# Performance work log

Measured on AMD Instinct MI355X. Metric: run time of the kernel, lower is better.

## Reference

```python
import jax, jax.numpy as jnp
import numpy as np

N = 50000
E = 640000
H = 128

def setup_inputs() -> dict:
    key = jax.random.key(0)
    ks = jax.random.split(key, 12)
    def lin(kw, fan_in, fan_out):
        # torch nn.Linear default init: U(-1/sqrt(fan_in), 1/sqrt(fan_in))
        lim = 1.0 / np.sqrt(fan_in)
        return jax.random.uniform(kw, (fan_in, fan_out), jnp.float32, -lim, lim)
    def bias(kb, fan_in, fan_out):
        lim = 1.0 / np.sqrt(fan_in)
        return jax.random.uniform(kb, (fan_out,), jnp.float32, -lim, lim)
    return {
        "x": jax.random.normal(ks[0], (N, H), jnp.float32),
        "pos": jax.random.normal(ks[1], (N, 3), jnp.float32),
        "edge_index": jax.random.randint(ks[2], (2, E), 0, N, jnp.int64),
        "msg_w1": lin(ks[3], 2 * H + 1, H), "msg_b1": bias(ks[4], 2 * H + 1, H),
        "msg_w2": lin(ks[5], H, H),         "msg_b2": bias(ks[6], H, H),
        "upd_w1": lin(ks[7], 2 * H, H),     "upd_b1": bias(ks[8], 2 * H, H),
        "upd_w2": lin(ks[9], H, H),         "upd_b2": bias(ks[10], H, H),
    }

def reference(x, pos, edge_index, msg_w1, msg_b1, msg_w2, msg_b2,
              upd_w1, upd_b1, upd_w2, upd_b2):
    send, rec = edge_index[0], edge_index[1]
    # pairwise distance per edge: [E]
    dist = jnp.linalg.norm(pos[send] - pos[rec], axis=1)
    # per-edge state: [E, 2H+1]
    state = jnp.concatenate([x[send], x[rec], dist[:, None]], axis=1)
    # message MLP: Linear -> SiLU -> Linear -> SiLU
    h = jax.nn.silu(state @ msg_w1 + msg_b1)
    message = jax.nn.silu(h @ msg_w2 + msg_b2)  # [E, H]
    # scatter-add into receiving nodes: [N, H]
    aggr = jax.ops.segment_sum(message, rec, num_segments=x.shape[0])
    # update MLP: Linear -> SiLU -> Linear
    u = jax.nn.silu(jnp.concatenate([x, aggr], axis=1) @ upd_w1 + upd_b1)
    update = u @ upd_w2 + upd_b2
    return update
```

## Files before the change

### kernel.cpp

```cpp
#include <hip/hip_runtime.h>
#include <math.h>

#define H 128

typedef unsigned short u16;
typedef unsigned int u32;
typedef __attribute__((ext_vector_type(4))) u32 u32x4;
typedef __attribute__((ext_vector_type(8))) __bf16 bf16x8;
typedef __attribute__((ext_vector_type(4))) float f32x4;
typedef __attribute__((ext_vector_type(16))) float f32x16;

union Frag { u32x4 u; bf16x8 b; };

__device__ __forceinline__ u32 pack2(float lo, float hi) {
    union { __bf16 b[2]; u32 u; } v;
    v.b[0] = (__bf16)lo; v.b[1] = (__bf16)hi;
    return v.u;
}
__device__ __forceinline__ float bflo(u32 w) {
    union { u32 i; float f; } v; v.i = w << 16; return v.f;
}
__device__ __forceinline__ float bfhi(u32 w) {
    union { u32 i; float f; } v; v.i = w & 0xffff0000u; return v.f;
}
__device__ __forceinline__ float silu(float v) {
    float e = __expf(-v);
    return v * __builtin_amdgcn_rcpf(1.0f + e);
}
__device__ __forceinline__ bf16x8 f8frag(float4 lo, float4 hi) {
    Frag f;
    f.u = (u32x4){pack2(lo.x, lo.y), pack2(lo.z, lo.w),
                  pack2(hi.x, hi.y), pack2(hi.z, hi.w)};
    return f.b;
}
__device__ __forceinline__ f32x16 mfma(bf16x8 a, bf16x8 b, f32x16 c) {
    return __builtin_amdgcn_mfma_f32_32x32x16_bf16(a, b, c, 0, 0, 0);
}
__device__ __forceinline__ f32x4 mfma16(bf16x8 a, bf16x8 b, f32x4 c) {
    return __builtin_amdgcn_mfma_f32_16x16x32_bf16(a, b, c, 0, 0, 0);
}
#define DPP_RADD(v, ctrl) \
    (v) += __int_as_float(__builtin_amdgcn_update_dpp(0, __float_as_int(v), (ctrl), 0xf, 0xf, 1))

__global__ void prep_kernel(const float* __restrict__ mw1, const float* __restrict__ mb1,
                            const float* __restrict__ mw2, const float* __restrict__ mb2,
                            const float* __restrict__ uw1, const float* __restrict__ ub1,
                            const float* __restrict__ uw2, const float* __restrict__ ub2,
                            u32* __restrict__ ws) {
    int t = blockIdx.x * blockDim.x + threadIdx.x;
    if (t >= 15936) return;
    if (t >= 15872) {
        int i = t - 15872;
        ws[63488 + i] = pack2(mw1[256 * H + 2 * i], mw1[256 * H + 2 * i + 1]);
        return;
    }
    if (t >= 13312) {
        int slot = t - 13312;
        int lane = slot & 63, fb = slot >> 6;
        int kb = fb >> 3, mt = fb & 7;
        int m = mt * 16 + (lane & 15);
        int quad = lane >> 4;
        u32 out[4];
        #pragma unroll
        for (int p = 0; p < 4; ++p) {
            float v[2];
            #pragma unroll
            for (int h = 0; h < 2; ++h) {
                int k = kb * 32 + quad * 8 + p * 2 + h;
                float val = 0.0f;
                if (k < 128)       val = mw2[(size_t)k * H + m];
                else if (k == 128) val = mb2[m];
                v[h] = val;
            }
            out[p] = pack2(v[0], v[1]);
        }
        u32* dst = ws + 53248 + (size_t)slot * 4;
        dst[0] = out[0]; dst[1] = out[1]; dst[2] = out[2]; dst[3] = out[3];
        return;
    }
    const float *W, *s0, *s1;
    int nK, slot, base;
    if (t < 4352)       { W = mw1; s0 = mw1 + 256 * H; s1 = mb1; nK = 256; slot = t;         base = 0;     }
    else if (t < 6656)  { W = mw2; s0 = mb2; s1 = nullptr;       nK = 128; slot = t - 4352;  base = 17408; }
    else if (t < 11008) { W = uw1; s0 = ub1; s1 = nullptr;       nK = 256; slot = t - 6656;  base = 26624; }
    else                { W = uw2; s0 = ub2; s1 = nullptr;       nK = 128; slot = t - 11008; base = 44032; }
    int lane = slot & 63, fb = slot >> 6;
    int ct, kb;
    if (nK == 256) { ct = fb / 17; kb = fb % 17; }
    else           { ct = fb / 9;  kb = fb % 9;  }
    int m = ct * 32 + (lane & 31);
    int q = lane >> 5;
    u32 out[4];
    #pragma unroll
    for (int p = 0; p < 4; ++p) {
        float v[2];
        #pragma unroll
        for (int h = 0; h < 2; ++h) {
            int k = kb * 16 + q * 8 + p * 2 + h;
            float val = 0.0f;
            if (k < nK)            val = W[(size_t)k * H + m];
            else if (k == nK)      val = s0 ? s0[m] : 0.0f;
            else if (k == nK + 1)  val = s1 ? s1[m] : 0.0f;
            v[h] = val;
        }
        out[p] = pack2(v[0], v[1]);
    }
    u32* dst = ws + base + (size_t)slot * 4;
    dst[0] = out[0]; dst[1] = out[1]; dst[2] = out[2]; dst[3] = out[3];
}

__global__ __launch_bounds__(256, 2) void front_kernel(
    const float* __restrict__ x, const u32* __restrict__ mw1s,
    u32* __restrict__ Pb, u32* __restrict__ Qb,
    const float* __restrict__ pos, const int* __restrict__ ei,
    int* __restrict__ deg, int2* __restrict__ bucket,
    int N, int E, int nIter, int PQB, int BKB)
{
    const int b = blockIdx.x;
    if (b < 2 * PQB) {
        const int isQ = (b >= PQB);
        const int bb = isQ ? (b - PQB) : b;
        const int kbBase = isQ ? 8 : 0;
        u32* outb = isQ ? Qb : Pb;

        const int lane = threadIdx.x & 63;
        const int q = lane >> 5, el = lane & 31;
        const int gw  = bb * 4 + (threadIdx.x >> 6);
        const int gws = PQB * 4;

        for (int it = gw; it < nIter; it += gws) {
            const int nA = it * 32 + el;
            const int ncA = (nA < N) ? nA : (N - 1);
            const float* xA = x + (size_t)ncA * H;

            f32x16 acc[4];
            #pragma unroll
            for (int ct = 0; ct < 4; ++ct) acc[ct] = (f32x16)0.0f;

            #pragma unroll
            for (int kb = 0; kb < 8; ++kb) {
                const int f = kb * 16 + q * 8;
                bf16x8 bA = f8frag(*(const float4*)(xA + f), *(const float4*)(xA + f + 4));
                #pragma unroll
                for (int ct = 0; ct < 4; ++ct) {
                    Frag a; a.u = *(const u32x4*)&mw1s[((size_t)(ct * 17 + kbBase + kb) * 64 + lane) * 4];
                    acc[ct] = mfma(a.b, bA, acc[ct]);
                }
            }
            if (isQ) {
                Frag bp; bp.u = (u32x4){0, 0, 0, 0};
                if (q == 0) bp.u.x = pack2(0.0f, 1.0f);
                #pragma unroll
                for (int ct = 0; ct < 4; ++ct) {
                    Frag a; a.u = *(const u32x4*)&mw1s[((size_t)(ct * 17 + 16) * 64 + lane) * 4];
                    acc[ct] = mfma(a.b, bp.b, acc[ct]);
                }
            }
            if (nA < N) {
                u32* prow = outb + (size_t)nA * 64;
                #pragma unroll
                for (int ct = 0; ct < 4; ++ct)
                    #pragma unroll
                    for (int g = 0; g < 4; ++g) {
                        u32 a = pack2(acc[ct][4*g + 0], acc[ct][4*g + 1]);
                        u32 bb2 = pack2(acc[ct][4*g + 2], acc[ct][4*g + 3]);
                        *(uint2*)(prow + ct * 16 + 4 * g + 2 * q) = make_uint2(a, bb2);
                    }
            }
        }
    } else {
        const int bb = b - 2 * PQB;
        for (int e = bb * 256 + (int)threadIdx.x; e < E; e += BKB * 256) {
            const int s = ei[e];
            const int r = ei[E + e];
            const float dx = pos[s*3]   - pos[r*3];
            const float dy = pos[s*3+1] - pos[r*3+1];
            const float dz = pos[s*3+2] - pos[r*3+2];
            const float dist = sqrtf(dx*dx + dy*dy + dz*dz);
            int slot = atomicAdd(&deg[r], 1);
            if (slot < 64) bucket[(size_t)r * 64 + slot] = make_int2(s, __float_as_int(dist));
        }
    }
}

__global__ __launch_bounds__(256, 3) void aggregate_kernel(
    const u32* __restrict__ Pbf, const u32* __restrict__ Qbf,
    const u32* __restrict__ wdp, const u32* __restrict__ ws16,
    const float* __restrict__ mb2,
    const int* __restrict__ deg, const int2* __restrict__ bucket,
    float* __restrict__ out, int N)
{
    __shared__ u32x4 af[2048];
    __shared__ float b2s[128];
    __shared__ u32x4 wds[16];
    for (int i = threadIdx.x; i < 2048; i += 256) af[i] = ((const u32x4*)ws16)[i];
    for (int i = threadIdx.x; i < 128; i += 256) b2s[i] = mb2[i];
    if (threadIdx.x < 16) wds[threadIdx.x] = ((const u32x4*)wdp)[threadIdx.x];
    __syncthreads();

    const int lane = threadIdx.x & 63;
    const int quad = lane >> 4, col = lane & 15;

    const int gw  = blockIdx.x * 4 + (threadIdx.x >> 6);
    const int gws = gridDim.x * 4;

    for (int n = gw; n < N; n += gws) {
        int dn = deg[n]; dn = (dn > 64) ? 64 : dn;
        const int nt = (dn + 15) >> 4;
        const u32x4* Qrow = (const u32x4*)(Qbf + (size_t)n * 64);

        f32x4 sum[8];
        #pragma unroll
        for (int mt = 0; mt < 8; ++mt) sum[mt] = (f32x4){0.f, 0.f, 0.f, 0.f};

        for (int t = 0; t < nt; ++t) {
            const int eIdx = t * 16 + col;
            const bool valid = eIdx < dn;
            const int eC = valid ? eIdx : (dn - 1);
            const int2 rec = bucket[(size_t)n * 64 + eC];
            const u32x4* Prow = (const u32x4*)(Pbf + (size_t)rec.x * 64);
            const float dist = __int_as_float(rec.y);

            f32x4 acc[8];
            #pragma unroll
            for (int mt = 0; mt < 8; ++mt)
                acc[mt] = *(const f32x4*)&b2s[mt * 16 + quad * 4];

            #pragma unroll 2
            for (int kb = 0; kb < 4; ++kb) {
                const u32x4 pc = Prow[kb * 4 + quad];
                const u32x4 qc = Qrow[kb * 4 + quad];
                const u32x4 wc = wds[kb * 4 + quad];
                const float v0 = silu(bflo(pc.x) + bflo(qc.x) + dist * bflo(wc.x));
                const float v1 = silu(bfhi(pc.x) + bfhi(qc.x) + dist * bfhi(wc.x));
                const float v2 = silu(bflo(pc.y) + bflo(qc.y) + dist * bflo(wc.y));
                const float v3 = silu(bfhi(pc.y) + bfhi(qc.y) + dist * bfhi(wc.y));
                const float v4 = silu(bflo(pc.z) + bflo(qc.z) + dist * bflo(wc.z));
                const float v5 = silu(bfhi(pc.z) + bfhi(qc.z) + dist * bfhi(wc.z));
                const float v6 = silu(bflo(pc.w) + bflo(qc.w) + dist * bflo(wc.w));
                const float v7 = silu(bfhi(pc.w) + bfhi(qc.w) + dist * bfhi(wc.w));
                Frag bf;
                bf.u = (u32x4){pack2(v0, v1), pack2(v2, v3), pack2(v4, v5), pack2(v6, v7)};
                if (!valid) bf.u = (u32x4){0, 0, 0, 0};
                #pragma unroll
                for (int mt = 0; mt < 8; ++mt) {
                    Frag a; a.u = af[(kb * 8 + mt) * 64 + lane];
                    acc[mt] = mfma16(a.b, bf.b, acc[mt]);
                }
            }
            #pragma unroll
            for (int mt = 0; mt < 8; ++mt) {
                sum[mt][0] += valid ? silu(acc[mt][0]) : 0.0f;
                sum[mt][1] += valid ? silu(acc[mt][1]) : 0.0f;
                sum[mt][2] += valid ? silu(acc[mt][2]) : 0.0f;
                sum[mt][3] += valid ? silu(acc[mt][3]) : 0.0f;
            }
        }

        #pragma unroll
        for (int mt = 0; mt < 8; ++mt)
            #pragma unroll
            for (int r = 0; r < 4; ++r) {
                float v = sum[mt][r];
                DPP_RADD(v, 0x128);
                DPP_RADD(v, 0x124);
                DPP_RADD(v, 0x122);
                DPP_RADD(v, 0x121);
                sum[mt][r] = v;
            }
        if (col == 0) {
            float* orow = out + (size_t)n * H;
            #pragma unroll
            for (int mt = 0; mt < 8; ++mt) {
                float4 v = { sum[mt][0], sum[mt][1], sum[mt][2], sum[mt][3] };
                *(float4*)(orow + mt * 16 + quad * 4) = v;
            }
        }
    }
}

__global__ __launch_bounds__(256, 2) void node1_kernel(
    const float* __restrict__ x, const float* __restrict__ aggr,
    const u32* __restrict__ ws, u32* __restrict__ Hb, int N, int nIter)
{
    __shared__ u32 lds[16384];
    const u32* wsl1 = ws + 26624;
    {
        const u32x4* src = (const u32x4*)wsl1;
        u32x4* dst = (u32x4*)lds;
        for (int i = threadIdx.x; i < 4096; i += 256) {
            int ln = i & 63, fb = i >> 6, ct = fb >> 4, kb = fb & 15;
            dst[i] = src[(ct * 17 + kb) * 64 + ln];
        }
    }
    __syncthreads();

    const int lane = threadIdx.x & 63;
    const int q = lane >> 5, el = lane & 31;
    const int gw  = blockIdx.x * 4 + (threadIdx.x >> 6);
    const int gws = gridDim.x * 4;

    for (int it = gw; it < nIter; it += gws) {
        const int nA = it * 32 + el;
        const int ncA = (nA < N) ? nA : (N - 1);
        const float* xA = x + (size_t)ncA * H;
        const float* gA = aggr + (size_t)ncA * H;

        f32x16 acc[4];
        #pragma unroll
        for (int ct = 0; ct < 4; ++ct) acc[ct] = (f32x16)0.0f;

        #pragma unroll
        for (int kb = 0; kb < 16; ++kb) {
            const int f = kb * 16 + q * 8;
            const float* pA = (f < H) ? (xA + f) : (gA + f - H);
            bf16x8 bA = f8frag(*(const float4*)pA, *(const float4*)(pA + 4));
            #pragma unroll
            for (int ct = 0; ct < 4; ++ct) {
                Frag a; a.u = *(const u32x4*)&lds[((ct * 16 + kb) * 64 + lane) * 4];
                acc[ct] = mfma(a.b, bA, acc[ct]);
            }
        }
        {
            Frag bp; bp.u = (u32x4){0,0,0,0};
            if (q == 0) bp.u.x = 0x00003F80u;
            #pragma unroll
            for (int ct = 0; ct < 4; ++ct) {
                Frag a; a.u = *(const u32x4*)&wsl1[((size_t)(ct * 17 + 16) * 64 + lane) * 4];
                acc[ct] = mfma(a.b, bp.b, acc[ct]);
            }
        }
        if (nA < N) {
            u32* hrow = Hb + (size_t)nA * 64;
            #pragma unroll
            for (int ct = 0; ct < 4; ++ct)
                #pragma unroll
                for (int g = 0; g < 4; ++g) {
                    u32 a = pack2(silu(acc[ct][4*g + 0]), silu(acc[ct][4*g + 1]));
                    u32 b = pack2(silu(acc[ct][4*g + 2]), silu(acc[ct][4*g + 3]));
                    *(uint2*)(hrow + ct * 16 + 4 * g + 2 * q) = make_uint2(a, b);
                }
        }
    }
}

__global__ __launch_bounds__(256, 2) void node2_kernel(
    const u32* __restrict__ Hb, const u32* __restrict__ ws,
    float* __restrict__ out, int N, int nIter)
{
    const u32* wsl2 = ws + 44032;
    const int lane = threadIdx.x & 63;
    const int q = lane >> 5, el = lane & 31;
    const int gw  = blockIdx.x * 4 + (threadIdx.x >> 6);
    const int gws = gridDim.x * 4;

    for (int it = gw; it < nIter; it += gws) {
        const int nA = it * 32 + el;
        const int ncA = (nA < N) ? nA : (N - 1);
        const u32* hrow = Hb + (size_t)ncA * 64;

        f32x16 acc[4];
        #pragma unroll
        for (int ct = 0; ct < 4; ++ct) acc[ct] = (f32x16)0.0f;

        #pragma unroll
        for (int kb = 0; kb < 8; ++kb) {
            Frag hb; hb.u = *(const u32x4*)&hrow[kb * 8 + q * 4];
            #pragma unroll
            for (int ct = 0; ct < 4; ++ct) {
                Frag a; a.u = *(const u32x4*)&wsl2[((size_t)(ct * 9 + kb) * 64 + lane) * 4];
                acc[ct] = mfma(a.b, hb.b, acc[ct]);
            }
        }
        {
            Frag bf; bf.u = (u32x4){0,0,0,0};
            if (q == 0) bf.u.x = 0x00003F80u;
            #pragma unroll
            for (int ct = 0; ct < 4; ++ct) {
                Frag a; a.u = *(const u32x4*)&wsl2[((size_t)(ct * 9 + 8) * 64 + lane) * 4];
                acc[ct] = mfma(a.b, bf.b, acc[ct]);
            }
        }
        if (nA < N) {
            float* orow = out + (size_t)nA * H;
            #pragma unroll
            for (int ct = 0; ct < 4; ++ct)
                #pragma unroll
                for (int g = 0; g < 4; ++g) {
                    float4 v = { acc[ct][4*g + 0], acc[ct][4*g + 1],
                                 acc[ct][4*g + 2], acc[ct][4*g + 3] };
                    *(float4*)(orow + ct * 32 + 8 * g + 4 * q) = v;
                }
        }
    }
}

__global__ __launch_bounds__(256, 2) void edge_mfma(
    const float* __restrict__ x, const float* __restrict__ pos,
    const int* __restrict__ ei, const u32* __restrict__ ws,
    float* __restrict__ aggr, int E, int nIter)
{
    __shared__ u32 lds[16384];
    {
        const u32x4* src = (const u32x4*)ws;
        u32x4* dst = (u32x4*)lds;
        for (int i = threadIdx.x; i < 4096; i += 256) {
            int ln = i & 63, fb = i >> 6, ct = fb >> 4, kb = fb & 15;
            dst[i] = src[(ct * 17 + kb) * 64 + ln];
        }
    }
    __syncthreads();
    const u32* wsl1 = ws;
    const u32* wsl2 = ws + 17408;

    const int lane = threadIdx.x & 63;
    const int q = lane >> 5, el = lane & 31;
    const int gw  = blockIdx.x * 4 + (threadIdx.x >> 6);
    const int gws = gridDim.x * 4;

    for (int it = gw; it < nIter; it += gws) {
        const int e0 = it * 64;
        const int sA = ei[e0 + el],      rA = ei[E + e0 + el];
        const int sB = ei[e0 + 32 + el], rB = ei[E + e0 + 32 + el];
        float dA, dB;
        {
            float ax = pos[sA*3] - pos[rA*3], ay = pos[sA*3+1] - pos[rA*3+1], az = pos[sA*3+2] - pos[rA*3+2];
            dA = sqrtf(ax*ax + ay*ay + az*az);
            float bx = pos[sB*3] - pos[rB*3], by = pos[sB*3+1] - pos[rB*3+1], bz = pos[sB*3+2] - pos[rB*3+2];
            dB = sqrtf(bx*bx + by*by + bz*bz);
        }
        const float* xsA = x + (size_t)sA * H; const float* xrA = x + (size_t)rA * H;
        const float* xsB = x + (size_t)sB * H; const float* xrB = x + (size_t)rB * H;

        f32x16 acc[2][4];
        #pragma unroll
        for (int s = 0; s < 2; ++s)
            #pragma unroll
            for (int ct = 0; ct < 4; ++ct) acc[s][ct] = (f32x16)0.0f;

        #pragma unroll
        for (int kb = 0; kb < 16; ++kb) {
            const int f = kb * 16 + q * 8;
            const float* pA = (f < H) ? (xsA + f) : (xrA + f - H);
            const float* pB = (f < H) ? (xsB + f) : (xrB + f - H);
            bf16x8 bA = f8frag(*(const float4*)pA, *(const float4*)(pA + 4));
            bf16x8 bB = f8frag(*(const float4*)pB, *(const float4*)(pB + 4));
            #pragma unroll
            for (int ct = 0; ct < 4; ++ct) {
                Frag a; a.u = *(const u32x4*)&lds[((ct * 16 + kb) * 64 + lane) * 4];
                acc[0][ct] = mfma(a.b, bA, acc[0][ct]);
                acc[1][ct] = mfma(a.b, bB, acc[1][ct]);
            }
        }
        {
            Frag bA, bB;
            bA.u = (u32x4){0,0,0,0}; bB.u = (u32x4){0,0,0,0};
            if (q == 0) { bA.u.x = pack2(dA, 1.0f); bB.u.x = pack2(dB, 1.0f); }
            #pragma unroll
            for (int ct = 0; ct < 4; ++ct) {
                Frag a; a.u = *(const u32x4*)&wsl1[((size_t)(ct * 17 + 16) * 64 + lane) * 4];
                acc[0][ct] = mfma(a.b, bA.b, acc[0][ct]);
                acc[1][ct] = mfma(a.b, bB.b, acc[1][ct]);
            }
        }

        #pragma unroll
        for (int s = 0; s < 2; ++s) {
            const int ridx = s ? rB : rA;
            u32 hp[16][2];
            #pragma unroll
            for (int ct = 0; ct < 4; ++ct)
                #pragma unroll
                for (int g = 0; g < 4; ++g) {
                    hp[ct * 4 + g][0] = pack2(silu(acc[s][ct][4*g + 0]), silu(acc[s][ct][4*g + 1]));
                    hp[ct * 4 + g][1] = pack2(silu(acc[s][ct][4*g + 2]), silu(acc[s][ct][4*g + 3]));
                }

            f32x16 acc2[4];
            #pragma unroll
            for (int ct = 0; ct < 4; ++ct) acc2[ct] = (f32x16)0.0f;

            #pragma unroll
            for (int kb2 = 0; kb2 < 8; ++kb2) {
                const u32 e0v = hp[2 * kb2][0],     e1v = hp[2 * kb2][1];
                const u32 o0v = hp[2 * kb2 + 1][0], o1v = hp[2 * kb2 + 1][1];
                const u32 w0  = q ? o0v : e0v;
                const u32 w1v = q ? o1v : e1v;
                const u32 sv0 = q ? e0v : o0v;
                const u32 sv1 = q ? e1v : o1v;
                u32 r0 = (u32)__shfl((int)sv0, lane ^ 32);
                u32 r1 = (u32)__shfl((int)sv1, lane ^ 32);
                Frag bf;
                if (q == 0) bf.u = (u32x4){w0, w1v, r0, r1};
                else        bf.u = (u32x4){r0, r1, w0, w1v};
                #pragma unroll
                for (int ct2 = 0; ct2 < 4; ++ct2) {
                    Frag a; a.u = *(const u32x4*)&wsl2[((size_t)(ct2 * 9 + kb2) * 64 + lane) * 4];
                    acc2[ct2] = mfma(a.b, bf.b, acc2[ct2]);
                }
            }
            {
                Frag bf; bf.u = (u32x4){0,0,0,0};
                if (q == 0) bf.u.x = 0x00003F80u;
                #pragma unroll
                for (int ct2 = 0; ct2 < 4; ++ct2) {
                    Frag a; a.u = *(const u32x4*)&wsl2[((size_t)(ct2 * 9 + 8) * 64 + lane) * 4];
                    acc2[ct2] = mfma(a.b, bf.b, acc2[ct2]);
                }
            }
            float* arow = aggr + (size_t)ridx * H;
            #pragma unroll
            for (int ct2 = 0; ct2 < 4; ++ct2)
                #pragma unroll
                for (int r = 0; r < 16; ++r) {
                    int m = ct2 * 32 + (r & 3) + 8 * (r >> 2) + 4 * q;
                    atomicAdd(arow + m, silu(acc2[ct2][r]));
                }
        }
    }
}

extern "C" void kernel_launch(void* const* d_in, const int* in_sizes, int n_in,
                              void* d_out, int out_size, void* d_ws, size_t ws_size,
                              hipStream_t stream) {
    const float* x    = (const float*)d_in[0];
    const float* pos  = (const float*)d_in[1];
    const int*   ei   = (const int*)d_in[2];
    const float* mw1  = (const float*)d_in[3];
    const float* mb1  = (const float*)d_in[4];
    const float* mw2  = (const float*)d_in[5];
    const float* mb2  = (const float*)d_in[6];
    const float* uw1  = (const float*)d_in[7];
    const float* ub1  = (const float*)d_in[8];
    const float* uw2  = (const float*)d_in[9];
    const float* ub2  = (const float*)d_in[10];

    const int N = in_sizes[0] / H;
    const int E = in_sizes[2] / 2;

    const size_t FRAGS = 53248 + 10240 + 64;
    const size_t PO = FRAGS;
    const size_t QO = PO + (size_t)N * 64;
    const size_t DG = QO + (size_t)N * 64;
    const size_t BK = DG + (size_t)N;
    const size_t ENDu = BK + (size_t)N * 128;
    const size_t need_bytes = ENDu * 4;

    u32* ws = (u32*)d_ws;
    prep_kernel<<<63, 256, 0, stream>>>(mw1, mb1, mw2, mb2, uw1, ub1, uw2, ub2, ws);

    float* buf = (float*)d_out;
    const int nIter32 = (N + 31) / 32;

    if (ws_size >= need_bytes) {
        u32*   Pb   = ws + PO;
        u32*   Qb   = ws + QO;
        int*   deg  = (int*)(ws + DG);
        int2*  bkt  = (int2*)(ws + BK);

        hipMemsetAsync(deg, 0, (size_t)N * sizeof(int), stream);

        const int PQB = 392;
        const int BKB = 640;
        front_kernel<<<2 * PQB + BKB, 256, 0, stream>>>(
            x, ws, Pb, Qb, pos, ei, deg, bkt, N, E, nIter32, PQB, BKB);

        aggregate_kernel<<<768, 256, 0, stream>>>(Pb, Qb, ws + 63488, ws + 53248,
                                                  mb2, deg, bkt, buf, N);

        node1_kernel<<<512, 256, 0, stream>>>(x, buf, ws, Pb, N, nIter32);
        node2_kernel<<<512, 256, 0, stream>>>(Pb, ws, buf, N, nIter32);
    } else {
        hipMemsetAsync(buf, 0, (size_t)N * H * sizeof(float), stream);
        edge_mfma<<<512, 256, 0, stream>>>(x, pos, ei, ws, buf, E, E / 64);
        node1_kernel<<<512, 256, 0, stream>>>(x, buf, ws, ws + PO, N, nIter32);
        node2_kernel<<<512, 256, 0, stream>>>(ws + PO, ws, buf, N, nIter32);
    }
}
```

Baseline: 338.4 us.

## Precompute x-half of update layer in front kernel and store aggregate as bf16

Adds a third job to the front kernel that computes the x·upd_w1 half of the first update layer into a bf16 buffer, overlapping it with the edge bucketing work. The aggregate kernel now writes bf16 instead of fp32 into the output buffer. A slimmer node1 kernel multiplies only the aggregate half, adds the precomputed x term and applies SiLU. This cuts node1 work and aggregate traffic, but the partial product loses precision by being rounded to bf16.

```diff
diff --git a/kernel.cpp b/kernel.cpp
--- a/kernel.cpp
+++ b/kernel.cpp
@@ -110,18 +110,19 @@
 }
 
 __global__ __launch_bounds__(256, 2) void front_kernel(
-    const float* __restrict__ x, const u32* __restrict__ mw1s,
-    u32* __restrict__ Pb, u32* __restrict__ Qb,
+    const float* __restrict__ x, const u32* __restrict__ ws,
+    u32* __restrict__ Pb, u32* __restrict__ Qb, u32* __restrict__ Ub,
     const float* __restrict__ pos, const int* __restrict__ ei,
     int* __restrict__ deg, int2* __restrict__ bucket,
     int N, int E, int nIter, int PQB, int BKB)
 {
     const int b = blockIdx.x;
-    if (b < 2 * PQB) {
-        const int isQ = (b >= PQB);
-        const int bb = isQ ? (b - PQB) : b;
-        const int kbBase = isQ ? 8 : 0;
-        u32* outb = isQ ? Qb : Pb;
+    if (b < 3 * PQB) {
+        const int job = b / PQB;
+        const int bb = b - job * PQB;
+        const int kbBase = (job == 1) ? 8 : 0;
+        const u32* wt = (job == 2) ? (ws + 26624) : ws;
+        u32* outb = (job == 0) ? Pb : ((job == 1) ? Qb : Ub);
 
         const int lane = threadIdx.x & 63;
         const int q = lane >> 5, el = lane & 31;
@@ -143,16 +144,16 @@
                 bf16x8 bA = f8frag(*(const float4*)(xA + f), *(const float4*)(xA + f + 4));
                 #pragma unroll
                 for (int ct = 0; ct < 4; ++ct) {
-                    Frag a; a.u = *(const u32x4*)&mw1s[((size_t)(ct * 17 + kbBase + kb) * 64 + lane) * 4];
+                    Frag a; a.u = *(const u32x4*)&wt[((size_t)(ct * 17 + kbBase + kb) * 64 + lane) * 4];
                     acc[ct] = mfma(a.b, bA, acc[ct]);
                 }
             }
-            if (isQ) {
+            if (job == 1) {
                 Frag bp; bp.u = (u32x4){0, 0, 0, 0};
                 if (q == 0) bp.u.x = pack2(0.0f, 1.0f);
                 #pragma unroll
                 for (int ct = 0; ct < 4; ++ct) {
-                    Frag a; a.u = *(const u32x4*)&mw1s[((size_t)(ct * 17 + 16) * 64 + lane) * 4];
+                    Frag a; a.u = *(const u32x4*)&ws[((size_t)(ct * 17 + 16) * 64 + lane) * 4];
                     acc[ct] = mfma(a.b, bp.b, acc[ct]);
                 }
             }
@@ -169,7 +170,7 @@
             }
         }
     } else {
-        const int bb = b - 2 * PQB;
+        const int bb = b - 3 * PQB;
         for (int e = bb * 256 + (int)threadIdx.x; e < E; e += BKB * 256) {
             const int s = ei[e];
             const int r = ei[E + e];
@@ -188,7 +189,7 @@
     const u32* __restrict__ wdp, const u32* __restrict__ ws16,
     const float* __restrict__ mb2,
     const int* __restrict__ deg, const int2* __restrict__ bucket,
-    float* __restrict__ out, int N)
+    u32* __restrict__ aggrp, int N)
 {
     __shared__ u32x4 af[2048];
     __shared__ float b2s[128];
@@ -269,17 +270,84 @@
                 sum[mt][r] = v;
             }
         if (col == 0) {
-            float* orow = out + (size_t)n * H;
+            u32* orow = aggrp + (size_t)n * 64;
             #pragma unroll
             for (int mt = 0; mt < 8; ++mt) {
-                float4 v = { sum[mt][0], sum[mt][1], sum[mt][2], sum[mt][3] };
-                *(float4*)(orow + mt * 16 + quad * 4) = v;
-            }
-        }
-    }
-}
-
-__global__ __launch_bounds__(256, 2) void node1_kernel(
+                u32 a = pack2(sum[mt][0], sum[mt][1]);
+                u32 b = pack2(sum[mt][2], sum[mt][3]);
+                *(uint2*)(orow + mt * 8 + quad * 2) = make_uint2(a, b);
+            }
+        }
+    }
+}
+
+__global__ __launch_bounds__(256, 2) void node1_slim(
+    const u32* __restrict__ aggrp, const u32* __restrict__ Ub,
+    const u32* __restrict__ ws, u32* __restrict__ Hb, int N, int nIter)
+{
+    __shared__ u32 lds[8192];
+    const u32* wsl1 = ws + 26624;
+    {
+        const u32x4* src = (const u32x4*)wsl1;
+        u32x4* dst = (u32x4*)lds;
+        for (int i = threadIdx.x; i < 2048; i += 256) {
+            int ln = i & 63, fb = i >> 6, ct = fb >> 3, kb = fb & 7;
+            dst[i] = src[(ct * 17 + 8 + kb) * 64 + ln];
+        }
+    }
+    __syncthreads();
+
+    const int lane = threadIdx.x & 63;
+    const int q = lane >> 5, el = lane & 31;
+    const int gw  = blockIdx.x * 4 + (threadIdx.x >> 6);
+    const int gws = gridDim.x * 4;
+
+    for (int it = gw; it < nIter; it += gws) {
+        const int nA = it * 32 + el;
+        const int ncA = (nA < N) ? nA : (N - 1);
+        const u32* arow = aggrp + (size_t)ncA * 64;
+        const u32* Urow = Ub + (size_t)ncA * 64;
+
+        f32x16 acc[4];
+        #pragma unroll
+        for (int ct = 0; ct < 4; ++ct) acc[ct] = (f32x16)0.0f;
+
+        #pragma unroll
+        for (int kb = 0; kb < 8; ++kb) {
+            Frag hb; hb.u = *(const u32x4*)&arow[kb * 8 + q * 4];
+            #pragma unroll
+            for (int ct = 0; ct < 4; ++ct) {
+                Frag a; a.u = *(const u32x4*)&lds[((ct * 8 + kb) * 64 + lane) * 4];
+                acc[ct] = mfma(a.b, hb.b, acc[ct]);
+            }
+        }
+        {
+            Frag bp; bp.u = (u32x4){0,0,0,0};
+            if (q == 0) bp.u.x = 0x00003F80u;
+            #pragma unroll
+            for (int ct = 0; ct < 4; ++ct) {
+                Frag a; a.u = *(const u32x4*)&wsl1[((size_t)(ct * 17 + 16) * 64 + lane) * 4];
+                acc[ct] = mfma(a.b, bp.b, acc[ct]);
+            }
+        }
+        if (nA < N) {
+            u32* hrow = Hb + (size_t)nA * 64;
+            #pragma unroll
+            for (int ct = 0; ct < 4; ++ct)
+                #pragma unroll
+                for (int g = 0; g < 4; ++g) {
+                    uint2 uv = *(const uint2*)&Urow[ct * 16 + 4 * g + 2 * q];
+                    u32 a = pack2(silu(acc[ct][4*g + 0] + bflo(uv.x)),
+                                  silu(acc[ct][4*g + 1] + bfhi(uv.x)));
+                    u32 b = pack2(silu(acc[ct][4*g + 2] + bflo(uv.y)),
+                                  silu(acc[ct][4*g + 3] + bfhi(uv.y)));
+                    *(uint2*)(hrow + ct * 16 + 4 * g + 2 * q) = make_uint2(a, b);
+                }
+        }
+    }
+}
+
+__global__ __launch_bounds__(256, 2) void node1_full(
     const float* __restrict__ x, const float* __restrict__ aggr,
     const u32* __restrict__ ws, u32* __restrict__ Hb, int N, int nIter)
 {
@@ -550,30 +618,33 @@
     prep_kernel<<<63, 256, 0, stream>>>(mw1, mb1, mw2, mb2, uw1, ub1, uw2, ub2, ws);
 
     float* buf = (float*)d_out;
+    u32* bufu = (u32*)d_out;
     const int nIter32 = (N + 31) / 32;
 
     if (ws_size >= need_bytes) {
-        u32*   Pb   = ws + PO;
-        u32*   Qb   = ws + QO;
-        int*   deg  = (int*)(ws + DG);
-        int2*  bkt  = (int2*)(ws + BK);
+        u32*   Pb    = ws + PO;
+        u32*   Qb    = ws + QO;
+        int*   deg   = (int*)(ws + DG);
+        int2*  bkt   = (int2*)(ws + BK);
+        u32*   aggrp = bufu;
+        u32*   Ub    = bufu + (size_t)N * 64;
 
         hipMemsetAsync(deg, 0, (size_t)N * sizeof(int), stream);
 
         const int PQB = 392;
         const int BKB = 640;
-        front_kernel<<<2 * PQB + BKB, 256, 0, stream>>>(
-            x, ws, Pb, Qb, pos, ei, deg, bkt, N, E, nIter32, PQB, BKB);
+        front_kernel<<<3 * PQB + BKB, 256, 0, stream>>>(
+            x, ws, Pb, Qb, Ub, pos, ei, deg, bkt, N, E, nIter32, PQB, BKB);
 
         aggregate_kernel<<<768, 256, 0, stream>>>(Pb, Qb, ws + 63488, ws + 53248,
-                                                  mb2, deg, bkt, buf, N);
-
-        node1_kernel<<<512, 256, 0, stream>>>(x, buf, ws, Pb, N, nIter32);
+                                                  mb2, deg, bkt, aggrp, N);
+
+        node1_slim<<<512, 256, 0, stream>>>(aggrp, Ub, ws, Pb, N, nIter32);
         node2_kernel<<<512, 256, 0, stream>>>(Pb, ws, buf, N, nIter32);
     } else {
         hipMemsetAsync(buf, 0, (size_t)N * H * sizeof(float), stream);
         edge_mfma<<<512, 256, 0, stream>>>(x, pos, ei, ws, buf, E, E / 64);
-        node1_kernel<<<512, 256, 0, stream>>>(x, buf, ws, ws + PO, N, nIter32);
+        node1_full<<<512, 256, 0, stream>>>(x, buf, ws, ws + PO, N, nIter32);
         node2_kernel<<<512, 256, 0, stream>>>(ws + PO, ws, buf, N, nIter32);
     }
 }
```

Measured after the change: 332.2 us. Within noise of the previous version (-1.8%).
